# Optimization experiments

Measured on AMD Instinct MI355X. Metric: run time of the kernel, lower is better.

## Reference

```python
import jax, jax.numpy as jnp
import numpy as np

N_NODES = 100000
N_EDGES = 3200000
N_GRAPHS = 1024
K = 32  # total number of kernels (num_kernel1..4 = 8 each)


def setup_inputs() -> dict:
    key = jax.random.key(0)
    ks = jax.random.split(key, 20)
    inp = {
        'x': jax.random.normal(ks[0], (N_NODES, 5), jnp.float32),
        'p': jax.random.normal(ks[1], (N_NODES, 3), jnp.float32),
        'edge_attr': jax.random.normal(ks[2], (N_EDGES, 1), jnp.float32),
        'Wx0': jax.random.normal(ks[3], (5, K), jnp.float32) * 0.3,
        'Wx1': jax.random.normal(ks[4], (K, K), jnp.float32) * 0.1,
        'Wx2': jax.random.normal(ks[5], (K, K), jnp.float32) * 0.1,
        'Wp0': jax.random.normal(ks[6], (3, K), jnp.float32) * 0.3,
        'Wp1': jax.random.normal(ks[7], (3, K), jnp.float32) * 0.3,
        'Wp2': jax.random.normal(ks[8], (3, K), jnp.float32) * 0.3,
        'We0': jax.random.normal(ks[9], (1, K), jnp.float32) * 0.3,
        'We1': jax.random.normal(ks[10], (1, K), jnp.float32) * 0.3,
        'We2': jax.random.normal(ks[11], (1, K), jnp.float32) * 0.3,
        'b0': jax.random.normal(ks[12], (K,), jnp.float32) * 0.1,
        'b1': jax.random.normal(ks[13], (K,), jnp.float32) * 0.1,
        'b2': jax.random.normal(ks[14], (K,), jnp.float32) * 0.1,
        'Wh': jax.random.normal(ks[15], (K, 1), jnp.float32) * 0.1,
        'bh': jax.random.normal(ks[16], (1,), jnp.float32) * 0.1,
        'edge_index': jax.random.randint(ks[17], (2, N_EDGES), 0, N_NODES, jnp.int64 if jax.config.jax_enable_x64 else jnp.int32),
        'batch': jnp.sort(jax.random.randint(ks[18], (N_NODES,), 0, N_GRAPHS, jnp.int64 if jax.config.jax_enable_x64 else jnp.int32)),
    }
    return inp


def _gnn_forward(x, p, edge_attr, Wxs, Wps, Wes, bs, edge_index):
    src, dst = edge_index[0], edge_index[1]
    p_rel = p[src] - p[dst]                      # [E, 3] relative positions
    h = x
    for Wx, Wp, We, b in zip(Wxs, Wps, Wes, bs):
        # kernel similarity per edge: gather neighbor feats + geometry, score vs K kernels
        msg = jnp.tanh(h[src] @ Wx + p_rel @ Wp + edge_attr @ We + b)   # [E, K]
        sim_sc = jax.ops.segment_sum(msg, dst, num_segments=N_NODES)    # [N, K] node sim scores
        # MolGCN.propagate: message(sim_sc_j) with aggr='add'
        h = jax.ops.segment_sum(sim_sc[src], dst, num_segments=N_NODES)  # [N, K]
    return h


def reference(x, p, edge_attr, Wx0, Wx1, Wx2, Wp0, Wp1, Wp2, We0, We1, We2,
              b0, b1, b2, Wh, bh, edge_index, batch):
    h = _gnn_forward(x, p, edge_attr, (Wx0, Wx1, Wx2), (Wp0, Wp1, Wp2),
                     (We0, We1, We2), (b0, b1, b2), edge_index)
    # global_mean_pool over graphs
    sums = jax.ops.segment_sum(h, batch, num_segments=N_GRAPHS)          # [G, K]
    cnt = jax.ops.segment_sum(jnp.ones((N_NODES,), h.dtype), batch, num_segments=N_GRAPHS)
    graph_rep = sums / jnp.maximum(cnt, 1.0)[:, None]                    # [G, K]
    pred = graph_rep @ Wh + bh                                           # [G, 1]
    return (pred, graph_rep)
```

## Files before the change

kernel.cpp:

```cpp
#include <hip/hip_runtime.h>
#include <hip/hip_fp16.h>

#define K_DIM 32
#define BN 256
#define MAXBUCK 512
#define TANH_SCALE 2.8853900817779268f


__global__ void k_bcnt(const int* __restrict__ dst, int* __restrict__ bcnt,
                       int E, int nbuck) {
    __shared__ int h[MAXBUCK];
    for (int i = threadIdx.x; i < nbuck; i += blockDim.x) h[i] = 0;
    __syncthreads();
    for (int e = blockIdx.x * blockDim.x + threadIdx.x; e < E; e += gridDim.x * blockDim.x)
        atomicAdd(&h[dst[e] >> 8], 1);
    __syncthreads();
    for (int i = threadIdx.x; i < nbuck; i += blockDim.x)
        if (h[i]) atomicAdd(&bcnt[i], h[i]);
}

__global__ void k_bscan(const int* __restrict__ bcnt, int* __restrict__ boff,
                        int* __restrict__ gcur, int nbuck, int total) {
    __shared__ int sm[256];
    __shared__ int carry;
    int t = threadIdx.x;
    if (t == 0) carry = 0;
    __syncthreads();
    for (int base = 0; base < nbuck; base += 256) {
        int v = (base + t < nbuck) ? bcnt[base + t] : 0;
        sm[t] = v;
        __syncthreads();
        #pragma unroll
        for (int d = 1; d < 256; d <<= 1) {
            int tv = (t >= d) ? sm[t - d] : 0;
            __syncthreads();
            sm[t] += tv;
            __syncthreads();
        }
        int excl = carry + sm[t] - v;
        if (base + t < nbuck) { boff[base + t] = excl; gcur[base + t] = excl; }
        __syncthreads();
        if (t == 0) carry += sm[255];
        __syncthreads();
    }
    if (t == 0) boff[nbuck] = total;
}

__global__ void k_bscatter(const int* __restrict__ src, const int* __restrict__ dst,
                           const float* __restrict__ ea, int* __restrict__ gcur,
                           uint2* __restrict__ rec, int E, int nbuck) {
    __shared__ int lcnt[MAXBUCK];
    __shared__ int lbase[MAXBUCK];
    const int nb = gridDim.x;
    const long c0 = (long)E * blockIdx.x / nb;
    const long c1 = (long)E * (blockIdx.x + 1) / nb;
    for (int i = threadIdx.x; i < nbuck; i += blockDim.x) lcnt[i] = 0;
    __syncthreads();
    for (long e = c0 + threadIdx.x; e < c1; e += blockDim.x)
        atomicAdd(&lcnt[dst[e] >> 8], 1);
    __syncthreads();
    for (int i = threadIdx.x; i < nbuck; i += blockDim.x) {
        int c = lcnt[i];
        lbase[i] = c ? atomicAdd(&gcur[i], c) : 0;
    }
    __syncthreads();
    for (int i = threadIdx.x; i < nbuck; i += blockDim.x) lcnt[i] = 0;
    __syncthreads();
    for (long e = c0 + threadIdx.x; e < c1; e += blockDim.x) {
        int d = dst[e];
        int b = d >> 8;
        int rank = atomicAdd(&lcnt[b], 1);
        unsigned meta = ((unsigned)(d & 255) << 17) | (unsigned)src[e];
        rec[lbase[b] + rank] = make_uint2(meta, __float_as_uint(ea[e]));
    }
}

__global__ void k_blocal(const uint2* __restrict__ rec, uint2* __restrict__ rec2,
                         int* __restrict__ srcs2, const int* __restrict__ boff,
                         int* __restrict__ off, int N, int E) {
    __shared__ int cnt[BN];
    __shared__ int base[BN];
    __shared__ int sm[BN];
    const int b = blockIdx.x;
    const int tid = threadIdx.x;
    int e0 = boff[b], e1 = boff[b + 1];
    int tot = e1 - e0;
    cnt[tid] = 0;
    __syncthreads();
    for (int i = tid; i < tot; i += 256)
        atomicAdd(&cnt[rec[e0 + i].x >> 17], 1);
    __syncthreads();
    int v = cnt[tid];
    sm[tid] = v;
    __syncthreads();
    #pragma unroll
    for (int d = 1; d < 256; d <<= 1) {
        int tv = (tid >= d) ? sm[tid - d] : 0;
        __syncthreads();
        sm[tid] += tv;
        __syncthreads();
    }
    base[tid] = sm[tid] - v;
    int n = b * BN + tid;
    if (n < N) off[n] = e0 + base[tid];
    if (b == 0 && tid == 0) off[N] = E;
    cnt[tid] = 0;
    __syncthreads();
    for (int i = tid; i < tot; i += 256) {
        uint2 r = rec[e0 + i];
        int dl = r.x >> 17;
        int rank = atomicAdd(&cnt[dl], 1);
        int pos = e0 + base[dl] + rank;
        unsigned s = r.x & 0x1FFFFu;
        float eaf = __uint_as_float(r.y);
        __half eh = __float2half(eaf);
        unsigned hb = (unsigned)__half_as_ushort(eh);
        rec2[pos] = make_uint2(s, (hb << 16) | hb);
        srcs2[pos] = (int)s;
    }
}


__global__ void k_node_gemm5(const float* __restrict__ h, const float* __restrict__ p,
                             const float* __restrict__ Wx, const float* __restrict__ Wp,
                             __half* __restrict__ Mh, int n_nodes) {
    __shared__ float sWx[5 * 32];
    __shared__ float sWp[96];
    for (int i = threadIdx.x; i < 5 * 32; i += blockDim.x) sWx[i] = Wx[i] * TANH_SCALE;
    if (threadIdx.x < 96) sWp[threadIdx.x] = Wp[threadIdx.x] * TANH_SCALE;
    __syncthreads();
    const int k = threadIdx.x & 31;
    int n = blockIdx.x * (blockDim.x >> 5) + (threadIdx.x >> 5);
    if (n >= n_nodes) return;
    float hv = (k < 5) ? h[n * 5 + k] : 0.0f;
    float pv = (k < 3) ? p[n * 3 + k] : 0.0f;
    float acc = 0.0f;
    #pragma unroll
    for (int j = 0; j < 5; ++j) acc = fmaf(__shfl(hv, j, 32), sWx[j * 32 + k], acc);
    #pragma unroll
    for (int j = 0; j < 3; ++j) acc = fmaf(__shfl(pv, j, 32), sWp[j * 32 + k], acc);
    Mh[n * 32 + k] = __float2half(acc);
}

__global__ void k_edge_msg(const __half* __restrict__ Mh, const float* __restrict__ p,
                           const int* __restrict__ off, const uint2* __restrict__ rec,
                           const float* __restrict__ Wp, const float* __restrict__ We,
                           const float* __restrict__ bias,
                           __half* __restrict__ simh, int N) {
    __shared__ uint2 stage[8][32];
    const int l = threadIdx.x & 31;
    const int c = l & 15;
    const int q = l >> 4;
    const int grp = threadIdx.x >> 5;
    int n = blockIdx.x * 8 + grp;
    if (n >= N) return;

    const __half2* Mh2 = (const __half2*)Mh;

    float2 wef = ((const float2*)We)[c];
    __half2 we2 = __floats2half2_rn(wef.x * TANH_SCALE, wef.y * TANH_SCALE);
    float2 b2  = ((const float2*)bias)[c];
    float2 wp0 = ((const float2*)Wp)[c];
    float2 wp1 = ((const float2*)(Wp + 32))[c];
    float2 wp2 = ((const float2*)(Wp + 64))[c];
    float pn = (l < 3) ? p[n * 3 + l] : 0.0f;
    float pn0 = __shfl(pn, 0, 32), pn1 = __shfl(pn, 1, 32), pn2 = __shfl(pn, 2, 32);
    __half2 cnst2 = __floats2half2_rn(
        (b2.x - (pn0 * wp0.x + pn1 * wp1.x + pn2 * wp2.x)) * TANH_SCALE,
        (b2.y - (pn0 * wp0.y + pn1 * wp1.y + pn2 * wp2.y)) * TANH_SCALE);
    const __half2 one2  = __floats2half2_rn(1.0f, 1.0f);
    const __half2 zero2 = __floats2half2_rn(0.0f, 0.0f);

    float fx = 0.0f, fy = 0.0f;
    int e0 = off[n], e1 = off[n + 1];
    for (int base = e0; base < e1; base += 32) {
        int m = min(32, e1 - base);
        uint2 r = (l < m) ? rec[base + l] : make_uint2(0u, 0u);
        stage[grp][l] = r;
        __half2 acc2 = zero2;
        for (int j = 0; j < m; j += 16) {
            __half2 mv[8], av[8];
            #pragma unroll
            for (int u = 0; u < 8; ++u) {
                uint2 e = stage[grp][j + 2 * u + q];
                unsigned eb = e.y;
                av[u] = *(const __half2*)&eb;
                mv[u] = Mh2[e.x * 16 + c];
            }
            #pragma unroll
            for (int u = 0; u < 8; ++u) {
                __half2 arg = __hadd2(__hfma2(av[u], we2, cnst2), mv[u]);
                __half2 ex  = h2exp2(arg);
                __half2 rr  = h2rcp(__hadd2(ex, one2));
                rr = (j + 2 * u + q < m) ? rr : zero2;
                acc2 = __hadd2(acc2, rr);
            }
        }
        fx += __low2float(acc2);
        fy += __high2float(acc2);
    }
    fx += __shfl_xor(fx, 16, 32);
    fy += __shfl_xor(fy, 16, 32);
    float deg = (float)(e1 - e0);
    if (l < 16)
        ((__half2*)simh)[n * 16 + c] =
            __floats2half2_rn(fmaf(-2.0f, fx, deg), fmaf(-2.0f, fy, deg));
}

template <int FUSE>
__global__ void k_prop_gemm(const __half* __restrict__ simh, const int* __restrict__ off,
                            const int* __restrict__ srcs, const float* __restrict__ p,
                            const float* __restrict__ Wx, const float* __restrict__ Wp,
                            __half* __restrict__ outMh, float* __restrict__ outF,
                            int N) {
    __shared__ float sWx[1024];
    __shared__ int stageS[8][32];
    if (FUSE) {
        for (int i = threadIdx.x; i < 1024; i += blockDim.x) sWx[i] = Wx[i] * TANH_SCALE;
        __syncthreads();
    }
    const int l = threadIdx.x & 31;
    const int c = l & 15;
    const int q = l >> 4;
    const int grp = threadIdx.x >> 5;
    int n = blockIdx.x * 8 + grp;
    if (n >= N) return;

    const __half2* sim2 = (const __half2*)simh;
    const __half2 zero2 = __floats2half2_rn(0.0f, 0.0f);
    float fx = 0.0f, fy = 0.0f;
    int e0 = off[n], e1 = off[n + 1];
    for (int base = e0; base < e1; base += 32) {
        int m = min(32, e1 - base);
        stageS[grp][l] = (l < m) ? srcs[base + l] : 0;
        for (int j = 0; j < m; j += 16) {
            __half2 v[8];
            #pragma unroll
            for (int u = 0; u < 8; ++u) {
                int s = stageS[grp][j + 2 * u + q];
                v[u] = sim2[s * 16 + c];
            }
            #pragma unroll
            for (int u = 0; u < 8; ++u) {
                __half2 vz = (j + 2 * u + q < m) ? v[u] : zero2;
                fx += __low2float(vz);
                fy += __high2float(vz);
            }
        }
    }
    fx += __shfl_xor(fx, 16, 32);
    fy += __shfl_xor(fy, 16, 32);

    if (!FUSE) {
        if (l < 16) ((float2*)outF)[n * 16 + c] = make_float2(fx, fy);
        return;
    }
    float mm = 0.0f;
    #pragma unroll
    for (int i = 0; i < 16; ++i) {
        float hx = __shfl(fx, i, 32);
        float hy = __shfl(fy, i, 32);
        mm = fmaf(hx, sWx[(2 * i) * 32 + l], mm);
        mm = fmaf(hy, sWx[(2 * i + 1) * 32 + l], mm);
    }
    float pv = (l < 3) ? p[n * 3 + l] : 0.0f;
    float pp = __shfl(pv, 0, 32) * Wp[l] + __shfl(pv, 1, 32) * Wp[32 + l]
             + __shfl(pv, 2, 32) * Wp[64 + l];
    mm = fmaf(pp, TANH_SCALE, mm);
    outMh[n * 32 + l] = __float2half(mm);
}


__global__ void k_pool(const float* __restrict__ h, const int* __restrict__ batch,
                       const float* __restrict__ Wh, const float* __restrict__ bh,
                       float* __restrict__ out, int n_nodes, int n_graphs) {
    __shared__ int sLo, sHi;
    __shared__ float red[256];
    int g = blockIdx.x;
    if (threadIdx.x == 0) {
        int lo = 0, hi = n_nodes;
        while (lo < hi) { int m = (lo + hi) >> 1; if (batch[m] < g) lo = m + 1; else hi = m; }
        sLo = lo;
        lo = 0; hi = n_nodes; int g1 = g + 1;
        while (lo < hi) { int m = (lo + hi) >> 1; if (batch[m] < g1) lo = m + 1; else hi = m; }
        sHi = lo;
    }
    __syncthreads();
    int lo = sLo, hi = sHi;
    int k = threadIdx.x & 31, r = threadIdx.x >> 5;
    float acc = 0.0f;
    for (int n = lo + r; n < hi; n += 8) acc += h[n * 32 + k];
    red[threadIdx.x] = acc;
    __syncthreads();
    if (threadIdx.x < 32) {
        float s = 0.0f;
        #pragma unroll
        for (int r2 = 0; r2 < 8; ++r2) s += red[r2 * 32 + k];
        float c = (float)(hi - lo);
        float rep = s / fmaxf(c, 1.0f);
        out[n_graphs + g * 32 + k] = rep;
        float t = rep * Wh[k];
        #pragma unroll
        for (int d = 16; d > 0; d >>= 1) t += __shfl_down(t, d, 32);
        if (k == 0) out[g] = t + bh[0];
    }
}


extern "C" void kernel_launch(void* const* d_in, const int* in_sizes, int n_in,
                              void* d_out, int out_size, void* d_ws, size_t ws_size,
                              hipStream_t stream) {
    const float* x   = (const float*)d_in[0];
    const float* p   = (const float*)d_in[1];
    const float* ea  = (const float*)d_in[2];
    const float* Wx0 = (const float*)d_in[3];
    const float* Wx1 = (const float*)d_in[4];
    const float* Wx2 = (const float*)d_in[5];
    const float* Wp0 = (const float*)d_in[6];
    const float* Wp1 = (const float*)d_in[7];
    const float* Wp2 = (const float*)d_in[8];
    const float* We0 = (const float*)d_in[9];
    const float* We1 = (const float*)d_in[10];
    const float* We2 = (const float*)d_in[11];
    const float* b0  = (const float*)d_in[12];
    const float* b1  = (const float*)d_in[13];
    const float* b2  = (const float*)d_in[14];
    const float* Wh  = (const float*)d_in[15];
    const float* bh  = (const float*)d_in[16];
    const int* edge_index = (const int*)d_in[17];
    const int* batch      = (const int*)d_in[18];

    const int N = in_sizes[0] / 5;
    const int E = in_sizes[17] / 2;
    const int G = out_size / 33;
    const int nbuck = (N + BN - 1) / BN;

    const int* srcp = edge_index;
    const int* dstp = edge_index + E;

    char* w = (char*)d_ws;
    auto alloc = [&](size_t bytes) -> void* {
        void* r = (void*)w;
        w += (bytes + 255) & ~(size_t)255;
        return r;
    };
    int*    bcnt  = (int*)alloc((size_t)nbuck * 4);
    int*    boff  = (int*)alloc((size_t)(nbuck + 1) * 4);
    int*    gcur  = (int*)alloc((size_t)nbuck * 4);
    int*    off   = (int*)alloc((size_t)(N + 1) * 4);
    uint2*  rec   = (uint2*)alloc((size_t)E * 8);
    uint2*  rec2  = (uint2*)alloc((size_t)E * 8);
    int*    srcs2 = (int*)alloc((size_t)E * 4);
    __half* Mh    = (__half*)alloc((size_t)N * K_DIM * 2);
    __half* simh  = (__half*)alloc((size_t)N * K_DIM * 2);
    float*  hB    = (float*)alloc((size_t)N * K_DIM * 4);

    (void)hipMemsetAsync(bcnt, 0, (size_t)nbuck * 4, stream);
    k_bcnt<<<1024, 256, 0, stream>>>(dstp, bcnt, E, nbuck);
    k_bscan<<<1, 256, 0, stream>>>(bcnt, boff, gcur, nbuck, E);
    k_bscatter<<<256, 1024, 0, stream>>>(srcp, dstp, ea, gcur, rec, E, nbuck);
    k_blocal<<<nbuck, 256, 0, stream>>>(rec, rec2, srcs2, boff, off, N, E);

    const int NB = (N + 7) / 8;

    k_node_gemm5<<<NB, 256, 0, stream>>>(x, p, Wx0, Wp0, Mh, N);
    k_edge_msg<<<NB, 256, 0, stream>>>(Mh, p, off, rec2, Wp0, We0, b0, simh, N);
    k_prop_gemm<1><<<NB, 256, 0, stream>>>(simh, off, srcs2, p, Wx1, Wp1, Mh, nullptr, N);
    k_edge_msg<<<NB, 256, 0, stream>>>(Mh, p, off, rec2, Wp1, We1, b1, simh, N);
    k_prop_gemm<1><<<NB, 256, 0, stream>>>(simh, off, srcs2, p, Wx2, Wp2, Mh, nullptr, N);
    k_edge_msg<<<NB, 256, 0, stream>>>(Mh, p, off, rec2, Wp2, We2, b2, simh, N);
    k_prop_gemm<0><<<NB, 256, 0, stream>>>(simh, off, srcs2, p, nullptr, nullptr, nullptr, hB, N);

    k_pool<<<G, 256, 0, stream>>>(hB, batch, Wh, bh, (float*)d_out, N, G);
}
```

Before: 432.6 us.

## Use sentinel dummy node to drop masking, stage local sort in LDS, packed f32 adds

Padding lanes in the edge-message and propagation loops now point at an extra dummy node N. Its Mh row is +inf, so the sigmoid term becomes zero, and its simh row is zero. This removes the per-element validity select. The bucket-local sort in k_blocal writes into a shared-memory buffer first and then copies it out coalesced, replacing scattered global writes. The propagation accumulation uses v_pk_add_f32 inline asm. It adds one tiny init kernel, and the 10240-entry LDS buffer would overflow on a skewed bucket.

```diff
diff --git a/kernel.cpp b/kernel.cpp
--- a/kernel.cpp
+++ b/kernel.cpp
@@ -4,7 +4,14 @@
 #define K_DIM 32
 #define BN 256
 #define MAXBUCK 512
+#define CAP 10240
 #define TANH_SCALE 2.8853900817779268f
+
+typedef float f32x2 __attribute__((ext_vector_type(2)));
+
+__device__ __forceinline__ void pk_add(f32x2& acc, f32x2 v) {
+    asm("v_pk_add_f32 %0, %1, %0" : "+v"(acc) : "v"(v));
+}
 
 
 __global__ void k_bcnt(const int* __restrict__ dst, int* __restrict__ bcnt,
@@ -78,6 +85,7 @@
 __global__ void k_blocal(const uint2* __restrict__ rec, uint2* __restrict__ rec2,
                          int* __restrict__ srcs2, const int* __restrict__ boff,
                          int* __restrict__ off, int N, int E) {
+    __shared__ uint2 sB[CAP];
     __shared__ int cnt[BN];
     __shared__ int base[BN];
     __shared__ int sm[BN];
@@ -110,14 +118,23 @@
         uint2 r = rec[e0 + i];
         int dl = r.x >> 17;
         int rank = atomicAdd(&cnt[dl], 1);
-        int pos = e0 + base[dl] + rank;
         unsigned s = r.x & 0x1FFFFu;
         float eaf = __uint_as_float(r.y);
-        __half eh = __float2half(eaf);
-        unsigned hb = (unsigned)__half_as_ushort(eh);
-        rec2[pos] = make_uint2(s, (hb << 16) | hb);
-        srcs2[pos] = (int)s;
-    }
+        unsigned hb = (unsigned)__half_as_ushort(__float2half(eaf));
+        sB[base[dl] + rank] = make_uint2(s, (hb << 16) | hb);
+    }
+    __syncthreads();
+    for (int i = tid; i < tot; i += 256) {
+        uint2 r = sB[i];
+        rec2[e0 + i] = r;
+        srcs2[e0 + i] = (int)r.x;
+    }
+}
+
+__global__ void k_initdummy(__half* __restrict__ Mh, __half* __restrict__ simh, int N) {
+    int i = threadIdx.x;
+    Mh[N * 32 + i] = __ushort_as_half((unsigned short)0x7C00);
+    simh[N * 32 + i] = __ushort_as_half((unsigned short)0);
 }
 
 
@@ -175,7 +192,7 @@
     int e0 = off[n], e1 = off[n + 1];
     for (int base = e0; base < e1; base += 32) {
         int m = min(32, e1 - base);
-        uint2 r = (l < m) ? rec[base + l] : make_uint2(0u, 0u);
+        uint2 r = (l < m) ? rec[base + l] : make_uint2((unsigned)N, 0u);
         stage[grp][l] = r;
         __half2 acc2 = zero2;
         for (int j = 0; j < m; j += 16) {
@@ -192,7 +209,6 @@
                 __half2 arg = __hadd2(__hfma2(av[u], we2, cnst2), mv[u]);
                 __half2 ex  = h2exp2(arg);
                 __half2 rr  = h2rcp(__hadd2(ex, one2));
-                rr = (j + 2 * u + q < m) ? rr : zero2;
                 acc2 = __hadd2(acc2, rr);
             }
         }
@@ -227,12 +243,11 @@
     if (n >= N) return;
 
     const __half2* sim2 = (const __half2*)simh;
-    const __half2 zero2 = __floats2half2_rn(0.0f, 0.0f);
-    float fx = 0.0f, fy = 0.0f;
+    f32x2 facc = {0.0f, 0.0f};
     int e0 = off[n], e1 = off[n + 1];
     for (int base = e0; base < e1; base += 32) {
         int m = min(32, e1 - base);
-        stageS[grp][l] = (l < m) ? srcs[base + l] : 0;
+        stageS[grp][l] = (l < m) ? srcs[base + l] : N;
         for (int j = 0; j < m; j += 16) {
             __half2 v[8];
             #pragma unroll
@@ -242,12 +257,13 @@
             }
             #pragma unroll
             for (int u = 0; u < 8; ++u) {
-                __half2 vz = (j + 2 * u + q < m) ? v[u] : zero2;
-                fx += __low2float(vz);
-                fy += __high2float(vz);
+                float2 fv = __half22float2(v[u]);
+                f32x2 t = {fv.x, fv.y};
+                pk_add(facc, t);
             }
         }
     }
+    float fx = facc.x, fy = facc.y;
     fx += __shfl_xor(fx, 16, 32);
     fy += __shfl_xor(fy, 16, 32);
 
@@ -351,8 +367,8 @@
     uint2*  rec   = (uint2*)alloc((size_t)E * 8);
     uint2*  rec2  = (uint2*)alloc((size_t)E * 8);
     int*    srcs2 = (int*)alloc((size_t)E * 4);
-    __half* Mh    = (__half*)alloc((size_t)N * K_DIM * 2);
-    __half* simh  = (__half*)alloc((size_t)N * K_DIM * 2);
+    __half* Mh    = (__half*)alloc((size_t)(N + 1) * K_DIM * 2);
+    __half* simh  = (__half*)alloc((size_t)(N + 1) * K_DIM * 2);
     float*  hB    = (float*)alloc((size_t)N * K_DIM * 4);
 
     (void)hipMemsetAsync(bcnt, 0, (size_t)nbuck * 4, stream);
@@ -360,6 +376,7 @@
     k_bscan<<<1, 256, 0, stream>>>(bcnt, boff, gcur, nbuck, E);
     k_bscatter<<<256, 1024, 0, stream>>>(srcp, dstp, ea, gcur, rec, E, nbuck);
     k_blocal<<<nbuck, 256, 0, stream>>>(rec, rec2, srcs2, boff, off, N, E);
+    k_initdummy<<<1, 32, 0, stream>>>(Mh, simh, N);
 
     const int NB = (N + 7) / 8;
 
```

Result: faster. 398.3 us (-7.9%).
